# Kernel optimization log

Hardware: AMD Instinct MI355X
Metric: run time of the kernel (lower is better)

Reference implementation:

```python
import jax, jax.numpy as jnp
import numpy as np

B, N, DIM_IN, DIM_K, DIM_V, NH = 2, 2048, 1024, 1024, 1024, 16

def setup_inputs() -> dict:
    key = jax.random.key(0)
    ks = jax.random.split(key, 7)
    s_in = 1.0 / np.sqrt(DIM_IN)
    return {
        "x": jax.random.normal(ks[0], (B, N, DIM_IN), dtype=jnp.float32),
        "Wq": jax.random.uniform(ks[1], (DIM_IN, DIM_K), jnp.float32, -s_in, s_in),
        "bq": jax.random.uniform(ks[2], (DIM_K,), jnp.float32, -s_in, s_in),
        "Wk": jax.random.uniform(ks[3], (DIM_IN, DIM_K), jnp.float32, -s_in, s_in),
        "bk": jax.random.uniform(ks[4], (DIM_K,), jnp.float32, -s_in, s_in),
        "Wv": jax.random.uniform(ks[5], (DIM_IN, DIM_V), jnp.float32, -s_in, s_in),
        "bv": jax.random.uniform(ks[6], (DIM_V,), jnp.float32, -s_in, s_in),
    }

def reference(x, Wq, bq, Wk, bk, Wv, bv):
    b, n, _ = x.shape
    dk = DIM_K // NH
    dv = DIM_V // NH
    scale = 1.0 / np.sqrt(dk)
    # project and split heads: [b, nh, n, dk]
    q = (x @ Wq + bq).reshape(b, n, NH, dk).transpose(0, 2, 1, 3)
    k = (x @ Wk + bk).reshape(b, n, NH, dk).transpose(0, 2, 1, 3)
    v = (x @ Wv + bv).reshape(b, n, NH, dv).transpose(0, 2, 1, 3)
    dist = jnp.einsum('bhqd,bhkd->bhqk', q, k) * scale  # [b,nh,n,n]
    dist = jax.nn.softmax(dist, axis=-1)
    att = jnp.einsum('bhqk,bhkd->bhqd', dist, v)
    return att.transpose(0, 2, 1, 3).reshape(b, n, DIM_V)
```

## Files before the change

### kernel.cpp

```cpp
#include <hip/hip_runtime.h>

#define DI __device__ __forceinline__

typedef unsigned short u16;
typedef short short8 __attribute__((ext_vector_type(8)));
typedef float f32x2 __attribute__((ext_vector_type(2)));
typedef float f32x4 __attribute__((ext_vector_type(4)));
typedef float f32x16 __attribute__((ext_vector_type(16)));
typedef u16 u16x4 __attribute__((ext_vector_type(4)));
typedef unsigned u32x4 __attribute__((ext_vector_type(4)));
typedef int i32x2 __attribute__((ext_vector_type(2)));

DI u16 f2bf(float f){
    unsigned u = __builtin_bit_cast(unsigned, f);
    u += 0x7FFFu + ((u >> 16) & 1u);
    return (u16)(u >> 16);
}
DI float bf2f(u16 b){
    unsigned u = ((unsigned)b) << 16;
    return __builtin_bit_cast(float, u);
}

#if defined(__has_builtin)
#if __has_builtin(__builtin_amdgcn_global_load_lds)
#define HAS_GLL 1
#endif
#if __has_builtin(__builtin_amdgcn_exp2f)
#define HAS_EXP2 1
#endif
#if __has_builtin(__builtin_amdgcn_permlane32_swap)
#define HAS_PL32 1
#endif
#endif

DI void async16(u16* lds, const u16* g){
#ifdef HAS_GLL
    __builtin_amdgcn_global_load_lds(
        (const __attribute__((address_space(1))) unsigned int*)g,
        (__attribute__((address_space(3))) unsigned int*)lds, 16, 0, 0);
#else
    *(short8*)lds = *(const short8*)g;
#endif
}

DI float ex2(float x){
#ifdef HAS_EXP2
    return __builtin_amdgcn_exp2f(x);
#else
    return exp2f(x);
#endif
}

DI unsigned cvtpk(float lo, float hi){
    unsigned r;
    asm("v_cvt_pk_bf16_f32 %0, %1, %2" : "=v"(r) : "v"(lo), "v"(hi));
    return r;
}

DI i32x2 plswap(int a, int b){
#ifdef HAS_PL32
    return __builtin_amdgcn_permlane32_swap(a, b, false, false);
#else
    i32x2 r;
    int ax = __shfl_xor(a, 32), bx = __shfl_xor(b, 32);
    int hi = (threadIdx.x & 63) >> 5;
    r[0] = hi ? bx : a;
    r[1] = hi ? b : ax;
    return r;
#endif
}

#define SEQ   2048
#define DIN   1024
#define MTOT  4096
#define QSCALE 0.18033688011112042f

__global__ void k_prep(const float* __restrict__ x,
                       const float* __restrict__ Wq, const float* __restrict__ Wk,
                       const float* __restrict__ Wv,
                       u16* __restrict__ xb, u16* __restrict__ Wt3){
    __shared__ float t[32][33];
    int bid = blockIdx.x, tid = threadIdx.x;
    if (bid < 4096){
        int i = (bid * 256 + tid) * 4;
        f32x4 v = *(const f32x4*)(x + i);
        u16x4 o;
        #pragma unroll
        for (int j = 0; j < 4; j++) o[j] = f2bf(v[j]);
        *(u16x4*)(xb + i) = o;
    } else {
        int tb = bid - 4096;
        int z  = tb >> 10;
        int t2 = tb & 1023;
        const float* W = (z == 0) ? Wq : (z == 1) ? Wk : Wv;
        u16* Wt = Wt3 + (size_t)z * DIN * DIN;
        int tx = tid & 31, ty = tid >> 5;
        int n0 = (t2 & 31) * 32, k0 = (t2 >> 5) * 32;
        #pragma unroll
        for (int i = 0; i < 4; i++)
            t[ty + i*8][tx] = W[(size_t)(k0 + ty + i*8) * DIN + n0 + tx];
        __syncthreads();
        #pragma unroll
        for (int i = 0; i < 4; i++)
            Wt[(size_t)(n0 + ty + i*8) * DIN + k0 + tx] = f2bf(t[tx][ty + i*8]);
    }
}

__global__ __launch_bounds__(256, 3) void k_projf(const u16* __restrict__ A,
                                                  const u16* __restrict__ Wt3,
                                                  const float* __restrict__ bq,
                                                  const float* __restrict__ bk,
                                                  const float* __restrict__ bv,
                                                  u16* __restrict__ qb,
                                                  u16* __restrict__ kb,
                                                  u16* __restrict__ vtb){
    __shared__ __align__(16) u16 As[2][4096];
    __shared__ __align__(16) u16 Bs[2][4096];
    int tid = threadIdx.x;
    int l = tid & 63, w = tid >> 6;
    int lq = l & 15, lg = l >> 4;
    int wm = w >> 1, wn = w & 1;
    int by  = blockIdx.y;
    int mat = by >> 3;
    int m0 = blockIdx.x * 128, n0 = (by & 7) * 128;
    const u16* Bt = Wt3 + (size_t)mat * DIN * DIN;
    const float* bias = (mat == 0) ? bq : (mat == 1) ? bk : bv;

    int r0 = tid >> 2, c0 = (tid & 3) * 8;
    const u16* ap0 = A  + (size_t)(m0 + r0)      * DIN + c0;
    const u16* ap1 = A  + (size_t)(m0 + 64 + r0) * DIN + c0;
    const u16* bp0 = Bt + (size_t)(n0 + r0)      * DIN + c0;
    const u16* bp1 = Bt + (size_t)(n0 + 64 + r0) * DIN + c0;
    int d0 = tid * 8, d1 = 2048 + tid * 8;

#define PSTAGE(bi) {                                              \
    async16(&As[bi][d0], ap0); async16(&As[bi][d1], ap1);         \
    async16(&Bs[bi][d0], bp0); async16(&Bs[bi][d1], bp1);         \
    ap0 += 32; ap1 += 32; bp0 += 32; bp1 += 32; }

    f32x4 acc[4][4] = {};
    PSTAGE(0)

    for (int t = 0; t < 32; t++){
        int cur = t & 1;
        if (t + 1 < 32) PSTAGE(cur ^ 1)
        if (t == 0){
            asm volatile("s_waitcnt vmcnt(4)" ::: "memory");
            __builtin_amdgcn_s_barrier();
        }

        short8 af[4], bf[4];
        #pragma unroll
        for (int f = 0; f < 4; f++){
            af[f] = *(const short8*)&As[cur][(wm*64 + f*16 + lq) * 32 + lg * 8];
            bf[f] = *(const short8*)&Bs[cur][(wn*64 + f*16 + lq) * 32 + lg * 8];
        }
        __builtin_amdgcn_s_setprio(1);
        #pragma unroll
        for (int fm = 0; fm < 4; fm++)
            #pragma unroll
            for (int fn = 0; fn < 4; fn++)
                acc[fm][fn] = __builtin_amdgcn_mfma_f32_16x16x32_bf16(af[fm], bf[fn], acc[fm][fn], 0, 0, 0);
        __builtin_amdgcn_s_setprio(0);

        asm volatile("s_waitcnt vmcnt(0)" ::: "memory");
        __builtin_amdgcn_s_barrier();
    }
#undef PSTAGE

    if (mat == 2){
        for (int fn = 0; fn < 4; fn++){
            int cc = n0 + wn*64 + fn*16 + lq;
            float bvv = bias[cc];
            int hh = cc >> 6, d = cc & 63;
            for (int fm = 0; fm < 4; fm++){
                int mbase = m0 + wm*64 + fm*16 + lg*4;
                int b = mbase >> 11, n = mbase & 2047;
                u16x4 pv;
                for (int r = 0; r < 4; r++) pv[r] = f2bf(acc[fm][fn][r] + bvv);
                *(u16x4*)&vtb[((size_t)(b*16 + hh) * 64 + d) * SEQ + n] = pv;
            }
        }
    } else {
        u16* dst = (mat == 0) ? qb : kb;
        float sc = (mat == 0) ? QSCALE : 1.0f;
        u16* Cs = &As[0][0];
        float bvv[4];
        #pragma unroll
        for (int fn = 0; fn < 4; fn++) bvv[fn] = bias[n0 + wn*64 + fn*16 + lq];

        for (int fm = 0; fm < 4; fm++){
            __syncthreads();
            #pragma unroll
            for (int fn = 0; fn < 4; fn++){
                int c = wn*64 + fn*16 + lq;
                #pragma unroll
                for (int r = 0; r < 4; r++)
                    Cs[(wm*16 + lg*4 + r)*136 + c] = f2bf((acc[fm][fn][r] + bvv[fn]) * sc);
            }
            __syncthreads();
            #pragma unroll
            for (int j = 0; j < 2; j++){
                int wr = (tid >> 4) + j*16;
                int coloff = (tid & 15) * 8;
                int ng = m0 + (wr >> 4)*64 + fm*16 + (wr & 15);
                int b = ng >> 11, n = ng & 2047;
                int cg = n0 + coloff;
                int hh = cg >> 6, d = cg & 63;
                *(short8*)&dst[((size_t)(b*16 + hh) * SEQ + n) * 64 + d] =
                    *(const short8*)&Cs[wr*136 + coloff];
            }
        }
    }
}

#define MFMA32(a, b, c) __builtin_amdgcn_mfma_f32_32x32x16_bf16(a, b, c, 0, 0, 0)

#define MAKE_PA(dst, S, base) {                                   \
    unsigned a0 = cvtpk(S[base+0], S[base+1]);                    \
    unsigned a1 = cvtpk(S[base+2], S[base+3]);                    \
    unsigned b0 = cvtpk(S[base+4], S[base+5]);                    \
    unsigned b1 = cvtpk(S[base+6], S[base+7]);                    \
    i32x2 r0 = plswap((int)a0, (int)b0);                          \
    i32x2 r1 = plswap((int)a1, (int)b1);                          \
    u32x4 wv = {(unsigned)r0[0], (unsigned)r1[0],                 \
                (unsigned)r0[1], (unsigned)r1[1]};                \
    dst = __builtin_bit_cast(short8, wv); }

template<int SPLIT>
__global__ __launch_bounds__(256, 4) void k_attn(const u16* __restrict__ Q,
                                                 const u16* __restrict__ K,
                                                 const u16* __restrict__ Vt,
                                                 float* __restrict__ out,
                                                 u16* __restrict__ po,
                                                 float* __restrict__ mls){
    __shared__ __align__(16) u16 Ks[2][64 * 64];
    __shared__ __align__(16) u16 Vs[2][64 * 64];

    int tid = threadIdx.x, l = tid & 63, w = tid >> 6;
    int lq = l & 31, hi = l >> 5;
    int bh = blockIdx.y;
    int b = bh >> 4, h = bh & 15;
    int q0 = blockIdx.x * 128 + w * 32;
    int sp = blockIdx.z;
    int kvb = sp * (SEQ / SPLIT);
    const int NT = (SEQ / SPLIT) / 64;

    const u16* Qb = Q  + (size_t)bh * SEQ * 64;
    const u16* Kb = K  + (size_t)bh * SEQ * 64;
    const u16* Vb = Vt + (size_t)bh * 64 * SEQ;

    int row0 = tid >> 3;
    int c0   = (tid & 7) ^ (row0 & 7);
    const u16* kp0 = Kb + (size_t)(kvb + row0)      * 64 + c0 * 8;
    const u16* kp1 = Kb + (size_t)(kvb + row0 + 32) * 64 + c0 * 8;
    const u16* vp0 = Vb + (size_t)row0        * SEQ + kvb + c0 * 8;
    const u16* vp1 = Vb + (size_t)(row0 + 32) * SEQ + kvb + c0 * 8;
    int d0 = tid * 8, d1 = 2048 + tid * 8;

#define STAGE(bi) {                                               \
    async16(&Ks[bi][d0], kp0); async16(&Ks[bi][d1], kp1);         \
    async16(&Vs[bi][d0], vp0); async16(&Vs[bi][d1], vp1);         \
    kp0 += 64*64; kp1 += 64*64; vp0 += 64; vp1 += 64; }

    short8 qf[4];
    #pragma unroll
    for (int ks = 0; ks < 4; ks++)
        qf[ks] = *(const short8*)(Qb + (size_t)(q0 + lq) * 64 + ks*16 + hi*8);

    STAGE(0)

    float m = 0.f;
    float ls = 0.f;
    f32x16 o0 = {}, o1 = {};
    int rx = (lq & 7) << 4;

    for (int t = 0; t < NT; t++){
        int cur = t & 1;
        if (t + 1 < NT) STAGE(cur ^ 1)
        if (t == 0){
            if (NT > 1) asm volatile("s_waitcnt vmcnt(4)" ::: "memory");
            else        asm volatile("s_waitcnt vmcnt(0)" ::: "memory");
            __builtin_amdgcn_s_barrier();
        }

        const char* kB = (const char*)&Ks[cur][0];
        const char* vB = (const char*)&Vs[cur][0];

        f32x16 st0 = {}, st1 = {};
        __builtin_amdgcn_s_setprio(1);
        #pragma unroll
        for (int ks = 0; ks < 4; ks++){
            int cb = ((ks*2 + hi) << 4) ^ rx;
            short8 ka = *(const short8*)(kB + lq*128        + cb);
            short8 kb = *(const short8*)(kB + (32+lq)*128   + cb);
            st0 = MFMA32(ka, qf[ks], st0);
            st1 = MFMA32(kb, qf[ks], st1);
        }
        __builtin_amdgcn_s_setprio(0);

        if (m != 0.f){
            #pragma unroll
            for (int r = 0; r < 16; r++){ st0[r] -= m; st1[r] -= m; }
        }

        f32x2 ps = {0.f, 0.f};
        #pragma unroll
        for (int r = 0; r < 16; r += 2){
            st0[r]   = ex2(st0[r]);
            st0[r+1] = ex2(st0[r+1]);
            st1[r]   = ex2(st1[r]);
            st1[r+1] = ex2(st1[r+1]);
            f32x2 a = {st0[r], st0[r+1]};
            f32x2 c = {st1[r], st1[r+1]};
            ps += a + c;
        }
        float psum = ps[0] + ps[1];
        psum += __shfl_xor(psum, 32);

        short8 pa0, pa1, pa2, pa3;
        MAKE_PA(pa0, st0, 0)
        MAKE_PA(pa1, st0, 8)
        MAKE_PA(pa2, st1, 0)
        MAKE_PA(pa3, st1, 8)

        __builtin_amdgcn_s_setprio(1);
        #pragma unroll
        for (int kct = 0; kct < 4; kct++){
            short8 pf = (kct == 0) ? pa0 : (kct == 1) ? pa1 : (kct == 2) ? pa2 : pa3;
            int cb = ((kct*2 + hi) << 4) ^ rx;
            short8 v0 = *(const short8*)(vB + lq*128      + cb);
            short8 v1 = *(const short8*)(vB + (32+lq)*128 + cb);
            o0 = MFMA32(pf, v0, o0);
            o1 = MFMA32(pf, v1, o1);
        }
        __builtin_amdgcn_s_setprio(0);

        ls += psum;
        if (__any(ls > 1.0e30f)){
            const float dn = 5.421010862427522e-20f;
            ls *= dn;
            #pragma unroll
            for (int r = 0; r < 16; r++){ o0[r] *= dn; o1[r] *= dn; }
            m += 64.f;
        }

        asm volatile("s_waitcnt vmcnt(0)" ::: "memory");
        __builtin_amdgcn_s_barrier();
    }

    if (SPLIT == 1){
        #pragma unroll
        for (int r = 0; r < 16; r++){
            int row = (r & 3) + 8*(r >> 2) + 4*hi;
            float inv = 1.0f / __shfl(ls, row);
            float* op = out + ((size_t)b * SEQ + (q0 + row)) * 1024 + h*64 + lq;
            op[0]  = o0[r] * inv;
            op[32] = o1[r] * inv;
        }
    } else {
        u16* pb = po + (size_t)sp * MTOT * 1024;
        #pragma unroll
        for (int r = 0; r < 16; r++){
            int row = (r & 3) + 8*(r >> 2) + 4*hi;
            u16* op = pb + ((size_t)b * SEQ + (q0 + row)) * 1024 + h*64 + lq;
            op[0]  = f2bf(o0[r]);
            op[32] = f2bf(o1[r]);
        }
        if (hi == 0){
            float* mp = mls + (((size_t)sp*32 + bh) * SEQ + (q0 + lq)) * 2;
            mp[0] = m; mp[1] = ls;
        }
    }
#undef STAGE
}

template<int S>
__global__ __launch_bounds__(256) void k_comb(const u16* __restrict__ po,
                                              const float* __restrict__ mls,
                                              float* __restrict__ out){
    size_t i = ((size_t)blockIdx.x * 256 + threadIdx.x) * 4;
    size_t row = i >> 10;
    int col = (int)(i & 1023);
    int b = (int)(row >> 11), n = (int)(row & 2047);
    int bh = b*16 + (col >> 6);

    float mv[S], lv[S], wv[S];
    float M = -INFINITY;
    #pragma unroll
    for (int s = 0; s < S; s++){
        const float* p = mls + (((size_t)s*32 + bh) * SEQ + n) * 2;
        mv[s] = p[0]; lv[s] = p[1];
        M = fmaxf(M, mv[s]);
    }
    float L = 0.f;
    #pragma unroll
    for (int s = 0; s < S; s++){ wv[s] = ex2(mv[s] - M); L += wv[s] * lv[s]; }
    float inv = 1.0f / L;
    f32x4 acc = {};
    #pragma unroll
    for (int s = 0; s < S; s++){
        u16x4 v = *(const u16x4*)(po + (size_t)s * MTOT * 1024 + i);
        #pragma unroll
        for (int j = 0; j < 4; j++) acc[j] += wv[s] * bf2f(v[j]);
    }
    acc *= inv;
    *(f32x4*)(out + i) = acc;
}

extern "C" void kernel_launch(void* const* d_in, const int* in_sizes, int n_in,
                              void* d_out, int out_size, void* d_ws, size_t ws_size,
                              hipStream_t stream){
    const float* x  = (const float*)d_in[0];
    const float* Wq = (const float*)d_in[1];
    const float* bq = (const float*)d_in[2];
    const float* Wk = (const float*)d_in[3];
    const float* bk = (const float*)d_in[4];
    const float* Wv = (const float*)d_in[5];
    const float* bv = (const float*)d_in[6];
    float* out = (float*)d_out;

    const size_t MB = (size_t)1 << 20;
    if (ws_size < 38 * MB) return;

    char* ws = (char*)d_ws;
    u16* xb   = (u16*)(ws);
    u16* wt3  = (u16*)(ws +  8 * MB);
    u16* qb   = (u16*)(ws + 14 * MB);
    u16* kb   = (u16*)(ws + 22 * MB);
    u16* vtb  = (u16*)(ws + 30 * MB);
    int S = (ws_size >= 38 * MB + 2 * 9 * MB) ? 2 : 1;
    u16* po    = (u16*)(ws + 38 * MB);
    float* mls = (float*)(ws + 38 * MB + (size_t)S * 8 * MB);

    k_prep<<<7168, 256, 0, stream>>>(x, Wq, Wk, Wv, xb, wt3);

    k_projf<<<dim3(32, 24), 256, 0, stream>>>(xb, wt3, bq, bk, bv, qb, kb, vtb);

    if (S == 2){
        k_attn<2><<<dim3(16, 32, 2), 256, 0, stream>>>(qb, kb, vtb, out, po, mls);
        k_comb<2><<<4096, 256, 0, stream>>>(po, mls, out);
    } else {
        k_attn<1><<<dim3(16, 32, 1), 256, 0, stream>>>(qb, kb, vtb, out, po, mls);
    }
}
```

Baseline: 97.44 us.

## Use two waves per projection block with larger per-wave tiles

The projection GEMM block drops from four waves to two, and each wave now computes a 128x64 tile instead of a 64x64 tile. Each wave gets more MFMA work per LDS fragment load, and the async copy loop and epilogue are rewritten for 128 threads. In exchange the block has fewer waves to hide latency, and the per-wave accumulator count doubles, which raises register pressure.

```diff
diff --git a/kernel.cpp b/kernel.cpp
--- a/kernel.cpp
+++ b/kernel.cpp
@@ -106,7 +106,7 @@
     }
 }
 
-__global__ __launch_bounds__(256, 3) void k_projf(const u16* __restrict__ A,
+__global__ __launch_bounds__(128, 2) void k_projf(const u16* __restrict__ A,
                                                   const u16* __restrict__ Wt3,
                                                   const float* __restrict__ bq,
                                                   const float* __restrict__ bk,
@@ -119,45 +119,54 @@
     int tid = threadIdx.x;
     int l = tid & 63, w = tid >> 6;
     int lq = l & 15, lg = l >> 4;
-    int wm = w >> 1, wn = w & 1;
+    int wn = w;
     int by  = blockIdx.y;
     int mat = by >> 3;
     int m0 = blockIdx.x * 128, n0 = (by & 7) * 128;
     const u16* Bt = Wt3 + (size_t)mat * DIN * DIN;
     const float* bias = (mat == 0) ? bq : (mat == 1) ? bk : bv;
 
-    int r0 = tid >> 2, c0 = (tid & 3) * 8;
-    const u16* ap0 = A  + (size_t)(m0 + r0)      * DIN + c0;
-    const u16* ap1 = A  + (size_t)(m0 + 64 + r0) * DIN + c0;
-    const u16* bp0 = Bt + (size_t)(n0 + r0)      * DIN + c0;
-    const u16* bp1 = Bt + (size_t)(n0 + 64 + r0) * DIN + c0;
-    int d0 = tid * 8, d1 = 2048 + tid * 8;
+    int r0 = tid >> 2, c0e = (tid & 3) * 8;
+    const u16* ap0 = A  + (size_t)(m0 + r0)      * DIN + c0e;
+    const u16* ap1 = A  + (size_t)(m0 + 32 + r0) * DIN + c0e;
+    const u16* ap2 = A  + (size_t)(m0 + 64 + r0) * DIN + c0e;
+    const u16* ap3 = A  + (size_t)(m0 + 96 + r0) * DIN + c0e;
+    const u16* bp0 = Bt + (size_t)(n0 + r0)      * DIN + c0e;
+    const u16* bp1 = Bt + (size_t)(n0 + 32 + r0) * DIN + c0e;
+    const u16* bp2 = Bt + (size_t)(n0 + 64 + r0) * DIN + c0e;
+    const u16* bp3 = Bt + (size_t)(n0 + 96 + r0) * DIN + c0e;
+    int d0 = tid * 8;
 
 #define PSTAGE(bi) {                                              \
-    async16(&As[bi][d0], ap0); async16(&As[bi][d1], ap1);         \
-    async16(&Bs[bi][d0], bp0); async16(&Bs[bi][d1], bp1);         \
-    ap0 += 32; ap1 += 32; bp0 += 32; bp1 += 32; }
-
-    f32x4 acc[4][4] = {};
+    async16(&As[bi][d0       ], ap0); async16(&As[bi][d0 + 1024], ap1); \
+    async16(&As[bi][d0 + 2048], ap2); async16(&As[bi][d0 + 3072], ap3); \
+    async16(&Bs[bi][d0       ], bp0); async16(&Bs[bi][d0 + 1024], bp1); \
+    async16(&Bs[bi][d0 + 2048], bp2); async16(&Bs[bi][d0 + 3072], bp3); \
+    ap0 += 32; ap1 += 32; ap2 += 32; ap3 += 32;                   \
+    bp0 += 32; bp1 += 32; bp2 += 32; bp3 += 32; }
+
+    f32x4 acc[8][4] = {};
     PSTAGE(0)
 
     for (int t = 0; t < 32; t++){
         int cur = t & 1;
         if (t + 1 < 32) PSTAGE(cur ^ 1)
         if (t == 0){
-            asm volatile("s_waitcnt vmcnt(4)" ::: "memory");
+            asm volatile("s_waitcnt vmcnt(8)" ::: "memory");
             __builtin_amdgcn_s_barrier();
         }
 
-        short8 af[4], bf[4];
-        #pragma unroll
-        for (int f = 0; f < 4; f++){
-            af[f] = *(const short8*)&As[cur][(wm*64 + f*16 + lq) * 32 + lg * 8];
+        short8 af[8], bf[4];
+        #pragma unroll
+        for (int f = 0; f < 8; f++)
+            af[f] = *(const short8*)&As[cur][(f*16 + lq) * 32 + lg * 8];
+        #pragma unroll
+        for (int f = 0; f < 4; f++)
             bf[f] = *(const short8*)&Bs[cur][(wn*64 + f*16 + lq) * 32 + lg * 8];
-        }
+
         __builtin_amdgcn_s_setprio(1);
         #pragma unroll
-        for (int fm = 0; fm < 4; fm++)
+        for (int fm = 0; fm < 8; fm++)
             #pragma unroll
             for (int fn = 0; fn < 4; fn++)
                 acc[fm][fn] = __builtin_amdgcn_mfma_f32_16x16x32_bf16(af[fm], bf[fn], acc[fm][fn], 0, 0, 0);
@@ -169,14 +178,17 @@
 #undef PSTAGE
 
     if (mat == 2){
+        #pragma unroll
         for (int fn = 0; fn < 4; fn++){
             int cc = n0 + wn*64 + fn*16 + lq;
             float bvv = bias[cc];
             int hh = cc >> 6, d = cc & 63;
-            for (int fm = 0; fm < 4; fm++){
-                int mbase = m0 + wm*64 + fm*16 + lg*4;
+            #pragma unroll
+            for (int fm = 0; fm < 8; fm++){
+                int mbase = m0 + fm*16 + lg*4;
                 int b = mbase >> 11, n = mbase & 2047;
                 u16x4 pv;
+                #pragma unroll
                 for (int r = 0; r < 4; r++) pv[r] = f2bf(acc[fm][fn][r] + bvv);
                 *(u16x4*)&vtb[((size_t)(b*16 + hh) * 64 + d) * SEQ + n] = pv;
             }
@@ -189,21 +201,21 @@
         #pragma unroll
         for (int fn = 0; fn < 4; fn++) bvv[fn] = bias[n0 + wn*64 + fn*16 + lq];
 
-        for (int fm = 0; fm < 4; fm++){
+        for (int fm = 0; fm < 8; fm++){
             __syncthreads();
             #pragma unroll
             for (int fn = 0; fn < 4; fn++){
                 int c = wn*64 + fn*16 + lq;
                 #pragma unroll
                 for (int r = 0; r < 4; r++)
-                    Cs[(wm*16 + lg*4 + r)*136 + c] = f2bf((acc[fm][fn][r] + bvv[fn]) * sc);
+                    Cs[(lg*4 + r)*136 + c] = f2bf((acc[fm][fn][r] + bvv[fn]) * sc);
             }
             __syncthreads();
             #pragma unroll
             for (int j = 0; j < 2; j++){
-                int wr = (tid >> 4) + j*16;
+                int wr = (tid >> 4) + j*8;
                 int coloff = (tid & 15) * 8;
-                int ng = m0 + (wr >> 4)*64 + fm*16 + (wr & 15);
+                int ng = m0 + fm*16 + wr;
                 int b = ng >> 11, n = ng & 2047;
                 int cg = n0 + coloff;
                 int hh = cg >> 6, d = cg & 63;
@@ -435,7 +447,7 @@
 
     k_prep<<<7168, 256, 0, stream>>>(x, Wq, Wk, Wv, xb, wt3);
 
-    k_projf<<<dim3(32, 24), 256, 0, stream>>>(xb, wt3, bq, bk, bv, qb, kb, vtb);
+    k_projf<<<dim3(32, 24), 128, 0, stream>>>(xb, wt3, bq, bk, bv, qb, kb, vtb);
 
     if (S == 2){
         k_attn<2><<<dim3(16, 32, 2), 256, 0, stream>>>(qb, kb, vtb, out, po, mls);
```

After: 99.91 us. 1.03x slower.

## Software-pipeline PV matmul one tile behind QK with triple-buffered V

Applied to the files above, without the earlier changes.

Restructures the attention loop so the P·V MFMAs for tile t-1 run at the start of iteration t, before the QK^T MFMAs and softmax for tile t. V gets a third LDS buffer so the previous tile's V stays valid while the next one is prefetched, and a drain step after the loop handles the last tile. The intent is to interleave the exp/convert work with independent matrix ops and so shorten the serial dependency chain. The rescale check moves ahead of P packing and also scales the current probabilities. This costs extra LDS, which may lower occupancy, and more live registers to hold pa0..pa3 across iterations.

```diff
diff --git a/kernel.cpp b/kernel.cpp
--- a/kernel.cpp
+++ b/kernel.cpp
@@ -234,8 +234,8 @@
                                                  float* __restrict__ out,
                                                  u16* __restrict__ po,
                                                  float* __restrict__ mls){
-    __shared__ __align__(16) u16 Ks[2][64 * 64];
-    __shared__ __align__(16) u16 Vs[2][64 * 64];
+    __shared__ __align__(16) u16 Ks[2][4096];
+    __shared__ __align__(16) u16 Vs[3][4096];
 
     int tid = threadIdx.x, l = tid & 63, w = tid >> 6;
     int lq = l & 31, hi = l >> 5;
@@ -258,35 +258,51 @@
     const u16* vp1 = Vb + (size_t)(row0 + 32) * SEQ + kvb + c0 * 8;
     int d0 = tid * 8, d1 = 2048 + tid * 8;
 
-#define STAGE(bi) {                                               \
+#define STAGEK(bi) {                                              \
     async16(&Ks[bi][d0], kp0); async16(&Ks[bi][d1], kp1);         \
+    kp0 += 64*64; kp1 += 64*64; }
+#define STAGEV(bi) {                                              \
     async16(&Vs[bi][d0], vp0); async16(&Vs[bi][d1], vp1);         \
-    kp0 += 64*64; kp1 += 64*64; vp0 += 64; vp1 += 64; }
+    vp0 += 64; vp1 += 64; }
 
     short8 qf[4];
     #pragma unroll
     for (int ks = 0; ks < 4; ks++)
         qf[ks] = *(const short8*)(Qb + (size_t)(q0 + lq) * 64 + ks*16 + hi*8);
 
-    STAGE(0)
+    STAGEK(0) STAGEV(0)
 
     float m = 0.f;
     float ls = 0.f;
     f32x16 o0 = {}, o1 = {};
+    short8 pa0, pa1, pa2, pa3;
     int rx = (lq & 7) << 4;
 
     for (int t = 0; t < NT; t++){
-        int cur = t & 1;
-        if (t + 1 < NT) STAGE(cur ^ 1)
+        int kc = t & 1;
+        if (t + 1 < NT){ STAGEK(kc ^ 1) STAGEV((t + 1) % 3) }
         if (t == 0){
             if (NT > 1) asm volatile("s_waitcnt vmcnt(4)" ::: "memory");
             else        asm volatile("s_waitcnt vmcnt(0)" ::: "memory");
             __builtin_amdgcn_s_barrier();
         }
 
-        const char* kB = (const char*)&Ks[cur][0];
-        const char* vB = (const char*)&Vs[cur][0];
-
+        if (t > 0){
+            const char* vB = (const char*)&Vs[(t + 2) % 3][0];
+            __builtin_amdgcn_s_setprio(1);
+            #pragma unroll
+            for (int kct = 0; kct < 4; kct++){
+                short8 pf = (kct == 0) ? pa0 : (kct == 1) ? pa1 : (kct == 2) ? pa2 : pa3;
+                int cb = ((kct*2 + hi) << 4) ^ rx;
+                short8 v0 = *(const short8*)(vB + lq*128      + cb);
+                short8 v1 = *(const short8*)(vB + (32+lq)*128 + cb);
+                o0 = MFMA32(pf, v0, o0);
+                o1 = MFMA32(pf, v1, o1);
+            }
+            __builtin_amdgcn_s_setprio(0);
+        }
+
+        const char* kB = (const char*)&Ks[kc][0];
         f32x16 st0 = {}, st1 = {};
         __builtin_amdgcn_s_setprio(1);
         #pragma unroll
@@ -318,12 +334,29 @@
         float psum = ps[0] + ps[1];
         psum += __shfl_xor(psum, 32);
 
-        short8 pa0, pa1, pa2, pa3;
+        if (__any(ls + psum > 1.0e30f)){
+            const float dn = 5.421010862427522e-20f;
+            ls *= dn; psum *= dn;
+            #pragma unroll
+            for (int r = 0; r < 16; r++){
+                o0[r] *= dn; o1[r] *= dn;
+                st0[r] *= dn; st1[r] *= dn;
+            }
+            m += 64.f;
+        }
+        ls += psum;
+
         MAKE_PA(pa0, st0, 0)
         MAKE_PA(pa1, st0, 8)
         MAKE_PA(pa2, st1, 0)
         MAKE_PA(pa3, st1, 8)
 
+        asm volatile("s_waitcnt vmcnt(0)" ::: "memory");
+        __builtin_amdgcn_s_barrier();
+    }
+
+    {
+        const char* vB = (const char*)&Vs[(NT + 2) % 3][0];
         __builtin_amdgcn_s_setprio(1);
         #pragma unroll
         for (int kct = 0; kct < 4; kct++){
@@ -335,18 +368,6 @@
             o1 = MFMA32(pf, v1, o1);
         }
         __builtin_amdgcn_s_setprio(0);
-
-        ls += psum;
-        if (__any(ls > 1.0e30f)){
-            const float dn = 5.421010862427522e-20f;
-            ls *= dn;
-            #pragma unroll
-            for (int r = 0; r < 16; r++){ o0[r] *= dn; o1[r] *= dn; }
-            m += 64.f;
-        }
-
-        asm volatile("s_waitcnt vmcnt(0)" ::: "memory");
-        __builtin_amdgcn_s_barrier();
     }
 
     if (SPLIT == 1){
@@ -372,7 +393,8 @@
             mp[0] = m; mp[1] = ls;
         }
     }
-#undef STAGE
+#undef STAGEK
+#undef STAGEV
 }
 
 template<int S>
```

Result: no change. 96.95 us (-0.5%).
